# Optimization experiments

Hardware: AMD Instinct MI355X
Metric: run time of the kernel (lower is better)

The kernel has to match this reference:

```python
import jax, jax.numpy as jnp
import numpy as np

EMBED_DIM = 32  # module-level constant used for the 1/sqrt(d) scale in the source
DROP_P = 0.2


def setup_inputs() -> dict:
    key = jax.random.key(0)
    kx, kq, kk, kv = jax.random.split(key, 4)
    B, T, C = 8, 4096, EMBED_DIM
    x = jax.random.normal(kx, (B, T, C), dtype=jnp.float32)
    Wq = jax.random.normal(kq, (C, C), dtype=jnp.float32) * (1.0 / np.sqrt(C))
    Wk = jax.random.normal(kk, (C, C), dtype=jnp.float32) * (1.0 / np.sqrt(C))
    Wv = jax.random.normal(kv, (C, C), dtype=jnp.float32) * (1.0 / np.sqrt(C))
    return {"x": x, "Wq": Wq, "Wk": Wk, "Wv": Wv}


def reference(x, Wq, Wk, Wv):
    B, T, C = x.shape
    # bias-free linear projections: y = x @ W.T (torch nn.Linear convention)
    q = jnp.einsum('btc,dc->btd', x, Wq)
    k = jnp.einsum('btc,dc->btd', x, Wk)
    v = jnp.einsum('btc,dc->btd', x, Wv)
    # scaled scores [B, T, T]
    att = jnp.einsum('btd,bsd->bts', q, k) / jnp.sqrt(jnp.float32(EMBED_DIM))
    causal = jnp.tril(jnp.ones((T, T), dtype=bool))
    att = jnp.where(causal, att, -jnp.inf)
    wei = jax.nn.softmax(att, axis=-1)
    # dropout on attention weights (training mode, p=0.2), deterministic key
    keep = jax.random.bernoulli(jax.random.key(42), 1.0 - DROP_P, wei.shape)
    wei = jnp.where(keep, wei / (1.0 - DROP_P), 0.0)
    return jnp.einsum('bts,bsd->btd', wei, v)
```

## Files before the change

### kernel.cpp

```cpp
#include <hip/hip_runtime.h>
#include <stdint.h>

#define BB 8
#define TTN 4096
#define CCH 32
#define KEEP_LT9 3435974144u

typedef __attribute__((ext_vector_type(8))) short bf16x8;
typedef __attribute__((ext_vector_type(4))) float f32x4;

union B8 { uint32_t u[4]; uint4 q; bf16x8 v; };

__device__ __forceinline__ uint32_t cvt_pk_bf16(float lo, float hi) {
    uint32_t d;
    asm("v_cvt_pk_bf16_f32 %0, %1, %2" : "=v"(d) : "v"(lo), "v"(hi));
    return d;
}

__device__ __forceinline__ float exp2_fast(float x) {
    float d;
    asm("v_exp_f32 %0, %1" : "=v"(d) : "v"(x));
    return d;
}

__device__ __forceinline__ uint32_t rotl32(uint32_t x, int r) {
    return __builtin_amdgcn_alignbit(x, x, 32 - r);
}

__device__ __forceinline__ void threefry4(uint32_t i0, uint32_t i1, uint32_t i2, uint32_t i3,
                                          uint32_t& o0, uint32_t& o1, uint32_t& o2, uint32_t& o3) {
    const uint32_t K2 = 42u ^ 0x1BD11BDAu;
    uint32_t a0 = 0u, a1 = 0u, a2 = 0u, a3 = 0u;
    uint32_t b0 = i0 + 42u, b1 = i1 + 42u, b2 = i2 + 42u, b3 = i3 + 42u;
#define R4(r)                                                                  \
    { a0 += b0; a1 += b1; a2 += b2; a3 += b3;                                  \
      b0 = rotl32(b0, (r)); b1 = rotl32(b1, (r));                              \
      b2 = rotl32(b2, (r)); b3 = rotl32(b3, (r));                              \
      b0 ^= a0; b1 ^= a1; b2 ^= a2; b3 ^= a3; }
#define INJ(da, db)                                                            \
    { a0 += (da); a1 += (da); a2 += (da); a3 += (da);                          \
      b0 += (db); b1 += (db); b2 += (db); b3 += (db); }
    R4(13) R4(15) R4(26) R4(6)
    INJ(42u, K2 + 1u)
    R4(17) R4(29) R4(16) R4(24)
    INJ(K2, 2u)
    R4(13) R4(15) R4(26) R4(6)
    INJ(0u, 42u + 3u)
    R4(17) R4(29) R4(16) R4(24)
    INJ(42u, K2 + 4u)
    R4(13) R4(15) R4(26) R4(6)
    INJ(K2, 5u)
#undef R4
#undef INJ
    o0 = a0 ^ b0; o1 = a1 ^ b1; o2 = a2 ^ b2; o3 = a3 ^ b3;
}

__global__ __launch_bounds__(256) void proj_qkv(const float* __restrict__ x,
                                                const float* __restrict__ Wq,
                                                const float* __restrict__ Wk,
                                                const float* __restrict__ Wv,
                                                float* __restrict__ Qf,
                                                uint16_t* __restrict__ Kb,
                                                uint16_t* __restrict__ Vt) {
    __shared__ float sW[3][CCH * CCH];
    __shared__ uint16_t vs[256][34];
    const int tid = threadIdx.x;
    for (int i = tid; i < CCH * CCH; i += 256) {
        sW[0][i] = Wq[i]; sW[1][i] = Wk[i]; sW[2][i] = Wv[i];
    }
    __syncthreads();
    const int row = blockIdx.x * 256 + tid;
    const float4* xp = reinterpret_cast<const float4*>(x + (size_t)row * CCH);
    float xr[CCH];
    #pragma unroll
    for (int i = 0; i < 8; ++i) {
        float4 t4 = xp[i];
        xr[4*i] = t4.x; xr[4*i+1] = t4.y; xr[4*i+2] = t4.z; xr[4*i+3] = t4.w;
    }
    const float scale = 0.2550348616f;
    #pragma unroll
    for (int mtx = 0; mtx < 3; ++mtx) {
        float o[CCH];
        #pragma unroll
        for (int d = 0; d < CCH; ++d) {
            float s0 = 0.f, s1 = 0.f, s2 = 0.f, s3 = 0.f;
            #pragma unroll
            for (int c = 0; c < CCH; c += 4) {
                s0 += xr[c]   * sW[mtx][d*CCH + c];
                s1 += xr[c+1] * sW[mtx][d*CCH + c+1];
                s2 += xr[c+2] * sW[mtx][d*CCH + c+2];
                s3 += xr[c+3] * sW[mtx][d*CCH + c+3];
            }
            o[d] = (s0 + s1) + (s2 + s3);
            if (mtx == 0) o[d] *= scale;
        }
        if (mtx == 0) {
            float4* op = reinterpret_cast<float4*>(Qf + (size_t)row * CCH);
            #pragma unroll
            for (int i = 0; i < 8; ++i)
                op[i] = make_float4(o[4*i], o[4*i+1], o[4*i+2], o[4*i+3]);
        } else if (mtx == 1) {
            uint32_t dw[16];
            #pragma unroll
            for (int k = 0; k < 16; ++k) dw[k] = cvt_pk_bf16(o[2*k], o[2*k+1]);
            uint4* kp = reinterpret_cast<uint4*>((char*)Kb + (size_t)row * 64);
            #pragma unroll
            for (int q = 0; q < 4; ++q)
                kp[q] = make_uint4(dw[4*q], dw[4*q+1], dw[4*q+2], dw[4*q+3]);
        } else {
            #pragma unroll
            for (int k = 0; k < 16; ++k)
                *reinterpret_cast<uint32_t*>(&vs[tid][2*k]) = cvt_pk_bf16(o[2*k], o[2*k+1]);
        }
    }
    __syncthreads();
    const int b = blockIdx.x >> 4, seg = blockIdx.x & 15;
    const int d = tid >> 3, part = tid & 7;
    uint32_t dw[16];
    #pragma unroll
    for (int k = 0; k < 16; ++k) {
        const uint32_t lo = vs[part*32 + 2*k][d];
        const uint32_t hi = vs[part*32 + 2*k + 1][d];
        dw[k] = lo | (hi << 16);
    }
    uint16_t* dst = Vt + (size_t)b * (CCH * TTN) + (size_t)d * TTN + seg * 256 + part * 32;
    uint4* dp = reinterpret_cast<uint4*>(dst);
    #pragma unroll
    for (int q = 0; q < 4; ++q)
        dp[q] = make_uint4(dw[4*q], dw[4*q+1], dw[4*q+2], dw[4*q+3]);
}

__global__ __launch_bounds__(256, 6) void attn_mfma(const float* __restrict__ Qf,
                                                    const uint16_t* __restrict__ Kb,
                                                    const uint16_t* __restrict__ Vt,
                                                    float* __restrict__ out) {
    __shared__ __align__(16) char smem[9984];

    const int j = blockIdx.x;
    const int b = j & 7;
    const int thalf = (j >> 3) & 1;
    const int tile = 127 - (j >> 4);

    const int w = threadIdx.x >> 6;
    const int lane = threadIdx.x & 63;
    const int tl = lane & 15;
    const int g = lane >> 4;
    const int slb = w * 32;
    const int tbase = tile * 32 + thalf * 16;
    const int t_g = tbase + tl;

    const float* qrow = Qf + ((size_t)b * TTN + t_g) * CCH + g * 8;
    const float4 qa = *reinterpret_cast<const float4*>(qrow);
    const float4 qb = *reinterpret_cast<const float4*>(qrow + 4);
    B8 qf;
    qf.u[0] = cvt_pk_bf16(qa.x, qa.y); qf.u[1] = cvt_pk_bf16(qa.z, qa.w);
    qf.u[2] = cvt_pk_bf16(qb.x, qb.y); qf.u[3] = cvt_pk_bf16(qb.z, qb.w);

    f32x4 acc0 = {0.f,0.f,0.f,0.f}, acc1 = {0.f,0.f,0.f,0.f};
    float m = -1e30f, l = 0.f;

    const char* Kbb = (const char*)Kb + (size_t)b * TTN * 64;
    const char* Vbb = (const char*)Vt + (size_t)b * CCH * TTN * 2;
    const uint32_t idxb = ((uint32_t)b << 24) | ((uint32_t)t_g << 12);

    const int nwin = ((tbase + 15) >> 7) + 1;

    float* mxex = reinterpret_cast<float*>(smem) + (w << 6);
    uint32_t* pex = reinterpret_cast<uint32_t*>(smem + 1024) + (w << 8);

    B8 kaA, kcA, vaA, vcA, kaB, kcB, vaB, vcB;
    uint32_t rA[8], rB[8];

#define LOADF(KA, KC, VA, VC, S0)                                              \
    {                                                                          \
        const int srow = (S0) + slb;                                           \
        KA.q = *reinterpret_cast<const uint4*>(Kbb + (size_t)(srow + tl) * 64 + g * 16); \
        KC.q = *reinterpret_cast<const uint4*>(Kbb + (size_t)(srow + 16 + tl) * 64 + g * 16); \
        VA.q = *reinterpret_cast<const uint4*>(Vbb + (size_t)tl * 8192 + (size_t)(srow + g * 8) * 2); \
        VC.q = *reinterpret_cast<const uint4*>(Vbb + (size_t)(16 + tl) * 8192 + (size_t)(srow + g * 8) * 2); \
    }
#define TF8(R, S0)                                                             \
    {                                                                          \
        const uint32_t ib = idxb | (uint32_t)((S0) + slb + 4 * g);             \
        threefry4(ib,       ib + 1u,  ib + 2u,  ib + 3u,  R[0], R[1], R[2], R[3]); \
        threefry4(ib + 16u, ib + 17u, ib + 18u, ib + 19u, R[4], R[5], R[6], R[7]); \
    }
#define SMAXPV(S0, TAIL)                                                       \
    {                                                                          \
        const f32x4 zz = {0.f,0.f,0.f,0.f};                                    \
        f32x4 d0 = __builtin_amdgcn_mfma_f32_16x16x32_bf16(kaA.v, qf.v, zz, 0, 0, 0); \
        f32x4 d1 = __builtin_amdgcn_mfma_f32_16x16x32_bf16(kcA.v, qf.v, zz, 0, 0, 0); \
        if (TAIL) {                                                            \
            const int sv = (S0) + slb + 4 * g;                                 \
            d0.x = (sv + 0  <= t_g) ? d0.x : -1e30f;                           \
            d0.y = (sv + 1  <= t_g) ? d0.y : -1e30f;                           \
            d0.z = (sv + 2  <= t_g) ? d0.z : -1e30f;                           \
            d0.w = (sv + 3  <= t_g) ? d0.w : -1e30f;                           \
            d1.x = (sv + 16 <= t_g) ? d1.x : -1e30f;                           \
            d1.y = (sv + 17 <= t_g) ? d1.y : -1e30f;                           \
            d1.z = (sv + 18 <= t_g) ? d1.z : -1e30f;                           \
            d1.w = (sv + 19 <= t_g) ? d1.w : -1e30f;                           \
        }                                                                      \
        float mx = fmaxf(fmaxf(fmaxf(d0.x, d0.y), fmaxf(d0.z, d0.w)),          \
                         fmaxf(fmaxf(d1.x, d1.y), fmaxf(d1.z, d1.w)));         \
        mxex[(tl << 2) + g] = mx;                           \
        const float4 m4 = *reinterpret_cast<const float4*>(mxex + (tl << 2));  \
        mx = fmaxf(fmaxf(m4.x, m4.y), fmaxf(m4.z, m4.w));                      \
        const bool up = mx > m + 11.5f;          \
        const float corr = up ? exp2_fast(m - mx) : 1.0f;                      \
        m = up ? mx : m;                                                       \
        l *= corr; acc0 *= corr; acc1 *= corr;                                 \
        float p0 = exp2_fast(d0.x - m), p1 = exp2_fast(d0.y - m);              \
        float p2 = exp2_fast(d0.z - m), p3 = exp2_fast(d0.w - m);              \
        float p4 = exp2_fast(d1.x - m), p5 = exp2_fast(d1.y - m);              \
        float p6 = exp2_fast(d1.z - m), p7 = exp2_fast(d1.w - m);              \
        if (TAIL) {                                                            \
            const float alive = ((S0) + slb <= t_g) ? 1.0f : 0.0f;             \
            p0 *= alive; p1 *= alive; p2 *= alive; p3 *= alive;                \
            p4 *= alive; p5 *= alive; p6 *= alive; p7 *= alive;                \
        }                                                                      \
        l += ((p0 + p1) + (p2 + p3)) + ((p4 + p5) + (p6 + p7));                \
        const float q0 = (rA[0] < KEEP_LT9) ? p0 : 0.f;                        \
        const float q1 = (rA[1] < KEEP_LT9) ? p1 : 0.f;                        \
        const float q2 = (rA[2] < KEEP_LT9) ? p2 : 0.f;                        \
        const float q3 = (rA[3] < KEEP_LT9) ? p3 : 0.f;                        \
        const float q4 = (rA[4] < KEEP_LT9) ? p4 : 0.f;                        \
        const float q5 = (rA[5] < KEEP_LT9) ? p5 : 0.f;                        \
        const float q6 = (rA[6] < KEEP_LT9) ? p6 : 0.f;                        \
        const float q7 = (rA[7] < KEEP_LT9) ? p7 : 0.f;                        \
        const uint32_t k00 = cvt_pk_bf16(q0, q1), k01 = cvt_pk_bf16(q2, q3);   \
        const uint32_t k10 = cvt_pk_bf16(q4, q5), k11 = cvt_pk_bf16(q6, q7);   \
        *reinterpret_cast<uint4*>(pex + (lane << 2)) = make_uint4(k00, k01, k10, k11); \
        const int srcA4 = (((g & 1) ? 32 : 0) + tl) << 2;                      \
        const int sel = (g >= 2) ? 2 : 0;                                      \
        const uint2 lo2 = *reinterpret_cast<const uint2*>(pex + srcA4 + sel);  \
        const uint2 hi2 = *reinterpret_cast<const uint2*>(pex + srcA4 + 64 + sel); \
        B8 pf;                                                                 \
        pf.u[0] = lo2.x; pf.u[1] = lo2.y; pf.u[2] = hi2.x; pf.u[3] = hi2.y;    \
        acc0 = __builtin_amdgcn_mfma_f32_16x16x32_bf16(vaA.v, pf.v, acc0, 0, 0, 0); \
        acc1 = __builtin_amdgcn_mfma_f32_16x16x32_bf16(vcA.v, pf.v, acc1, 0, 0, 0); \
    }

    LOADF(kaA, kcA, vaA, vcA, 0)
    TF8(rA, 0)
    #pragma unroll 1
    for (int win = 0; win < nwin - 1; ++win) {
        LOADF(kaB, kcB, vaB, vcB, (win + 1) << 7)
        TF8(rB, (win + 1) << 7)
        SMAXPV(win << 7, 0)
        kaA = kaB; kcA = kcB; vaA = vaB; vcA = vcB;
        #pragma unroll
        for (int i = 0; i < 8; ++i) rA[i] = rB[i];
    }
    {
        const int s0 = (nwin - 1) << 7;
        if (s0 + slb <= tbase + 15) SMAXPV(s0, 1)
    }
#undef SMAXPV
#undef TF8
#undef LOADF

    l += __shfl_xor(l, 16);
    l += __shfl_xor(l, 32);

#define SLOT(S) reinterpret_cast<float*>(smem + 5120 + (S) * 2432)
#define PUBLISH(SB)                                                            \
    {                                                                          \
        float* sb = (SB);                                                      \
        *reinterpret_cast<float4*>(sb + tl * 36 + 4 * g)      = make_float4(acc0.x, acc0.y, acc0.z, acc0.w); \
        *reinterpret_cast<float4*>(sb + tl * 36 + 16 + 4 * g) = make_float4(acc1.x, acc1.y, acc1.z, acc1.w); \
        if (g == 0) { sb[576 + 2 * tl] = m; sb[577 + 2 * tl] = l; }            \
    }
#define CONSUME(SB)                                                            \
    {                                                                          \
        const float* sb = (SB);                                                \
        const float m2 = sb[576 + 2 * tl], l2 = sb[577 + 2 * tl];              \
        const float4 x0 = *reinterpret_cast<const float4*>(sb + tl * 36 + 4 * g); \
        const float4 x1 = *reinterpret_cast<const float4*>(sb + tl * 36 + 16 + 4 * g); \
        const float mn = fmaxf(m, m2);                                         \
        const float ca = exp2_fast(m - mn), cb = exp2_fast(m2 - mn);           \
        l = l * ca + l2 * cb;                                                  \
        acc0.x = acc0.x * ca + x0.x * cb; acc0.y = acc0.y * ca + x0.y * cb;    \
        acc0.z = acc0.z * ca + x0.z * cb; acc0.w = acc0.w * ca + x0.w * cb;    \
        acc1.x = acc1.x * ca + x1.x * cb; acc1.y = acc1.y * ca + x1.y * cb;    \
        acc1.z = acc1.z * ca + x1.z * cb; acc1.w = acc1.w * ca + x1.w * cb;    \
        m = mn;                                                                \
    }
    if (w >= 2) PUBLISH(SLOT(w - 2))
    __syncthreads();
    if (w < 2) CONSUME(SLOT(w))
    __syncthreads();
    if (w == 1) PUBLISH(SLOT(0))
    __syncthreads();
    if (w == 0) {
        CONSUME(SLOT(0))
        const float inv = 1.0f / (0.8f * l);
        float* orow = out + ((size_t)b * TTN + t_g) * CCH;
        *reinterpret_cast<float4*>(orow + 4 * g) =
            make_float4(acc0.x * inv, acc0.y * inv, acc0.z * inv, acc0.w * inv);
        *reinterpret_cast<float4*>(orow + 16 + 4 * g) =
            make_float4(acc1.x * inv, acc1.y * inv, acc1.z * inv, acc1.w * inv);
    }
#undef SLOT
#undef PUBLISH
#undef CONSUME
}

extern "C" void kernel_launch(void* const* d_in, const int* in_sizes, int n_in,
                              void* d_out, int out_size, void* d_ws, size_t ws_size,
                              hipStream_t stream) {
    const float* x  = (const float*)d_in[0];
    const float* Wq = (const float*)d_in[1];
    const float* Wk = (const float*)d_in[2];
    const float* Wv = (const float*)d_in[3];
    float* outp = (float*)d_out;

    float*    Qf = (float*)d_ws;
    uint16_t* Kb = (uint16_t*)((char*)d_ws + 4194304);
    uint16_t* Vt = (uint16_t*)((char*)d_ws + 6291456);

    proj_qkv<<<(BB * TTN) / 256, 256, 0, stream>>>(x, Wq, Wk, Wv, Qf, Kb, Vt);
    attn_mfma<<<2048, 256, 0, stream>>>(Qf, Kb, Vt, outp);
}
```

Measured before the change: 164.7 us.

## Split KV windows across two segments, pair causal tiles per block, add merge kernel

```diff
diff --git a/kernel.cpp b/kernel.cpp
--- a/kernel.cpp
+++ b/kernel.cpp
@@ -130,46 +130,51 @@
         dp[q] = make_uint4(dw[4*q], dw[4*q+1], dw[4*q+2], dw[4*q+3]);
 }
 
-__global__ __launch_bounds__(256, 6) void attn_mfma(const float* __restrict__ Qf,
+__global__ __launch_bounds__(256, 8) void attn_mfma(const float* __restrict__ Qf,
                                                     const uint16_t* __restrict__ Kb,
                                                     const uint16_t* __restrict__ Vt,
-                                                    float* __restrict__ out) {
+                                                    float* __restrict__ pws) {
     __shared__ __align__(16) char smem[9984];
 
     const int j = blockIdx.x;
     const int b = j & 7;
-    const int thalf = (j >> 3) & 1;
-    const int tile = 127 - (j >> 4);
+    const int p = (j >> 3) & 63;
+    const int h = (j >> 9) & 1;
+    const int seg = (j >> 10) & 1;
 
     const int w = threadIdx.x >> 6;
     const int lane = threadIdx.x & 63;
     const int tl = lane & 15;
     const int g = lane >> 4;
     const int slb = w * 32;
-    const int tbase = tile * 32 + thalf * 16;
-    const int t_g = tbase + tl;
-
-    const float* qrow = Qf + ((size_t)b * TTN + t_g) * CCH + g * 8;
-    const float4 qa = *reinterpret_cast<const float4*>(qrow);
-    const float4 qb = *reinterpret_cast<const float4*>(qrow + 4);
-    B8 qf;
-    qf.u[0] = cvt_pk_bf16(qa.x, qa.y); qf.u[1] = cvt_pk_bf16(qa.z, qa.w);
-    qf.u[2] = cvt_pk_bf16(qb.x, qb.y); qf.u[3] = cvt_pk_bf16(qb.z, qb.w);
-
-    f32x4 acc0 = {0.f,0.f,0.f,0.f}, acc1 = {0.f,0.f,0.f,0.f};
-    float m = -1e30f, l = 0.f;
 
     const char* Kbb = (const char*)Kb + (size_t)b * TTN * 64;
     const char* Vbb = (const char*)Vt + (size_t)b * CCH * TTN * 2;
-    const uint32_t idxb = ((uint32_t)b << 24) | ((uint32_t)t_g << 12);
-
-    const int nwin = ((tbase + 15) >> 7) + 1;
 
     float* mxex = reinterpret_cast<float*>(smem) + (w << 6);
     uint32_t* pex = reinterpret_cast<uint32_t*>(smem + 1024) + (w << 8);
 
-    B8 kaA, kcA, vaA, vcA, kaB, kcB, vaB, vcB;
-    uint32_t rA[8], rB[8];
+    #pragma unroll 1
+    for (int leg = 0; leg < 2; ++leg) {
+        const int tile = leg ? (127 - p) : p;
+        const int th = leg ? (1 - h) : h;
+        const int tbase = tile * 32 + th * 16;
+        const int t_g = tbase + tl;
+        const int nwin = ((tbase + 15) >> 7) + 1;
+        const uint32_t idxb = ((uint32_t)b << 24) | ((uint32_t)t_g << 12);
+
+        const float* qrow = Qf + ((size_t)b * TTN + t_g) * CCH + g * 8;
+        const float4 qa = *reinterpret_cast<const float4*>(qrow);
+        const float4 qb = *reinterpret_cast<const float4*>(qrow + 4);
+        B8 qf;
+        qf.u[0] = cvt_pk_bf16(qa.x, qa.y); qf.u[1] = cvt_pk_bf16(qa.z, qa.w);
+        qf.u[2] = cvt_pk_bf16(qb.x, qb.y); qf.u[3] = cvt_pk_bf16(qb.z, qb.w);
+
+        f32x4 acc0 = {0.f,0.f,0.f,0.f}, acc1 = {0.f,0.f,0.f,0.f};
+        float m = -1e30f, l = 0.f;
+
+        B8 kaA, kcA, vaA, vcA, kaB, kcB, vaB, vcB;
+        uint32_t rA[8], rB[8];
 
 #define LOADF(KA, KC, VA, VC, S0)                                              \
     {                                                                          \
@@ -185,12 +190,13 @@
         threefry4(ib,       ib + 1u,  ib + 2u,  ib + 3u,  R[0], R[1], R[2], R[3]); \
         threefry4(ib + 16u, ib + 17u, ib + 18u, ib + 19u, R[4], R[5], R[6], R[7]); \
     }
-#define SMAXPV(S0, TAIL)                                                       \
+#define SMAXPV(KA, KC, VA, VC, R, S0, ISTAIL)                                  \
     {                                                                          \
         const f32x4 zz = {0.f,0.f,0.f,0.f};                                    \
-        f32x4 d0 = __builtin_amdgcn_mfma_f32_16x16x32_bf16(kaA.v, qf.v, zz, 0, 0, 0); \
-        f32x4 d1 = __builtin_amdgcn_mfma_f32_16x16x32_bf16(kcA.v, qf.v, zz, 0, 0, 0); \
-        if (TAIL) {                                                            \
+        f32x4 d0 = __builtin_amdgcn_mfma_f32_16x16x32_bf16(KA.v, qf.v, zz, 0, 0, 0); \
+        f32x4 d1 = __builtin_amdgcn_mfma_f32_16x16x32_bf16(KC.v, qf.v, zz, 0, 0, 0); \
+        const bool istail_ = (ISTAIL);                                         \
+        if (istail_) {                                                         \
             const int sv = (S0) + slb + 4 * g;                                 \
             d0.x = (sv + 0  <= t_g) ? d0.x : -1e30f;                           \
             d0.y = (sv + 1  <= t_g) ? d0.y : -1e30f;                           \
@@ -203,10 +209,10 @@
         }                                                                      \
         float mx = fmaxf(fmaxf(fmaxf(d0.x, d0.y), fmaxf(d0.z, d0.w)),          \
                          fmaxf(fmaxf(d1.x, d1.y), fmaxf(d1.z, d1.w)));         \
-        mxex[(tl << 2) + g] = mx;                           \
+        mxex[(tl << 2) + g] = mx;                                              \
         const float4 m4 = *reinterpret_cast<const float4*>(mxex + (tl << 2));  \
         mx = fmaxf(fmaxf(m4.x, m4.y), fmaxf(m4.z, m4.w));                      \
-        const bool up = mx > m + 11.5f;          \
+        const bool up = mx > m + 11.5f;                                        \
         const float corr = up ? exp2_fast(m - mx) : 1.0f;                      \
         m = up ? mx : m;                                                       \
         l *= corr; acc0 *= corr; acc1 *= corr;                                 \
@@ -214,20 +220,20 @@
         float p2 = exp2_fast(d0.z - m), p3 = exp2_fast(d0.w - m);              \
         float p4 = exp2_fast(d1.x - m), p5 = exp2_fast(d1.y - m);              \
         float p6 = exp2_fast(d1.z - m), p7 = exp2_fast(d1.w - m);              \
-        if (TAIL) {                                                            \
+        if (istail_) {                                                         \
             const float alive = ((S0) + slb <= t_g) ? 1.0f : 0.0f;             \
             p0 *= alive; p1 *= alive; p2 *= alive; p3 *= alive;                \
             p4 *= alive; p5 *= alive; p6 *= alive; p7 *= alive;                \
         }                                                                      \
         l += ((p0 + p1) + (p2 + p3)) + ((p4 + p5) + (p6 + p7));                \
-        const float q0 = (rA[0] < KEEP_LT9) ? p0 : 0.f;                        \
-        const float q1 = (rA[1] < KEEP_LT9) ? p1 : 0.f;                        \
-        const float q2 = (rA[2] < KEEP_LT9) ? p2 : 0.f;                        \
-        const float q3 = (rA[3] < KEEP_LT9) ? p3 : 0.f;                        \
-        const float q4 = (rA[4] < KEEP_LT9) ? p4 : 0.f;                        \
-        const float q5 = (rA[5] < KEEP_LT9) ? p5 : 0.f;                        \
-        const float q6 = (rA[6] < KEEP_LT9) ? p6 : 0.f;                        \
-        const float q7 = (rA[7] < KEEP_LT9) ? p7 : 0.f;                        \
+        const float q0 = (R[0] < KEEP_LT9) ? p0 : 0.f;                         \
+        const float q1 = (R[1] < KEEP_LT9) ? p1 : 0.f;                         \
+        const float q2 = (R[2] < KEEP_LT9) ? p2 : 0.f;                         \
+        const float q3 = (R[3] < KEEP_LT9) ? p3 : 0.f;                         \
+        const float q4 = (R[4] < KEEP_LT9) ? p4 : 0.f;                         \
+        const float q5 = (R[5] < KEEP_LT9) ? p5 : 0.f;                         \
+        const float q6 = (R[6] < KEEP_LT9) ? p6 : 0.f;                         \
+        const float q7 = (R[7] < KEEP_LT9) ? p7 : 0.f;                         \
         const uint32_t k00 = cvt_pk_bf16(q0, q1), k01 = cvt_pk_bf16(q2, q3);   \
         const uint32_t k10 = cvt_pk_bf16(q4, q5), k11 = cvt_pk_bf16(q6, q7);   \
         *reinterpret_cast<uint4*>(pex + (lane << 2)) = make_uint4(k00, k01, k10, k11); \
@@ -237,31 +243,42 @@
         const uint2 hi2 = *reinterpret_cast<const uint2*>(pex + srcA4 + 64 + sel); \
         B8 pf;                                                                 \
         pf.u[0] = lo2.x; pf.u[1] = lo2.y; pf.u[2] = hi2.x; pf.u[3] = hi2.y;    \
-        acc0 = __builtin_amdgcn_mfma_f32_16x16x32_bf16(vaA.v, pf.v, acc0, 0, 0, 0); \
-        acc1 = __builtin_amdgcn_mfma_f32_16x16x32_bf16(vcA.v, pf.v, acc1, 0, 0, 0); \
-    }
-
-    LOADF(kaA, kcA, vaA, vcA, 0)
-    TF8(rA, 0)
-    #pragma unroll 1
-    for (int win = 0; win < nwin - 1; ++win) {
-        LOADF(kaB, kcB, vaB, vcB, (win + 1) << 7)
-        TF8(rB, (win + 1) << 7)
-        SMAXPV(win << 7, 0)
-        kaA = kaB; kcA = kcB; vaA = vaB; vcA = vcB;
-        #pragma unroll
-        for (int i = 0; i < 8; ++i) rA[i] = rB[i];
-    }
-    {
-        const int s0 = (nwin - 1) << 7;
-        if (s0 + slb <= tbase + 15) SMAXPV(s0, 1)
-    }
+        acc0 = __builtin_amdgcn_mfma_f32_16x16x32_bf16(VA.v, pf.v, acc0, 0, 0, 0); \
+        acc1 = __builtin_amdgcn_mfma_f32_16x16x32_bf16(VC.v, pf.v, acc1, 0, 0, 0); \
+    }
+
+        int win = seg;
+        if (win < nwin) {
+            LOADF(kaA, kcA, vaA, vcA, win << 7)
+            TF8(rA, win << 7)
+            while (true) {
+                int nxt = win + 2;
+                if (nxt < nwin) {
+                    LOADF(kaB, kcB, vaB, vcB, nxt << 7)
+                    TF8(rB, nxt << 7)
+                    SMAXPV(kaA, kcA, vaA, vcA, rA, win << 7, win == nwin - 1)
+                } else {
+                    SMAXPV(kaA, kcA, vaA, vcA, rA, win << 7, win == nwin - 1)
+                    break;
+                }
+                win = nxt; nxt = win + 2;
+                if (nxt < nwin) {
+                    LOADF(kaA, kcA, vaA, vcA, nxt << 7)
+                    TF8(rA, nxt << 7)
+                    SMAXPV(kaB, kcB, vaB, vcB, rB, win << 7, win == nwin - 1)
+                } else {
+                    SMAXPV(kaB, kcB, vaB, vcB, rB, win << 7, win == nwin - 1)
+                    break;
+                }
+                win = nxt;
+            }
+        }
 #undef SMAXPV
 #undef TF8
 #undef LOADF
 
-    l += __shfl_xor(l, 16);
-    l += __shfl_xor(l, 32);
+        l += __shfl_xor(l, 16);
+        l += __shfl_xor(l, 32);
 
 #define SLOT(S) reinterpret_cast<float*>(smem + 5120 + (S) * 2432)
 #define PUBLISH(SB)                                                            \
@@ -286,24 +303,57 @@
         acc1.z = acc1.z * ca + x1.z * cb; acc1.w = acc1.w * ca + x1.w * cb;    \
         m = mn;                                                                \
     }
-    if (w >= 2) PUBLISH(SLOT(w - 2))
-    __syncthreads();
-    if (w < 2) CONSUME(SLOT(w))
-    __syncthreads();
-    if (w == 1) PUBLISH(SLOT(0))
-    __syncthreads();
-    if (w == 0) {
-        CONSUME(SLOT(0))
-        const float inv = 1.0f / (0.8f * l);
-        float* orow = out + ((size_t)b * TTN + t_g) * CCH;
-        *reinterpret_cast<float4*>(orow + 4 * g) =
-            make_float4(acc0.x * inv, acc0.y * inv, acc0.z * inv, acc0.w * inv);
-        *reinterpret_cast<float4*>(orow + 16 + 4 * g) =
-            make_float4(acc1.x * inv, acc1.y * inv, acc1.z * inv, acc1.w * inv);
-    }
+        __syncthreads();
+        if (w >= 2) PUBLISH(SLOT(w - 2))
+        __syncthreads();
+        if (w < 2) CONSUME(SLOT(w))
+        __syncthreads();
+        if (w == 1) PUBLISH(SLOT(0))
+        __syncthreads();
+        if (w == 0) {
+            CONSUME(SLOT(0))
+            const int gi = (b << 8) + (tile << 1) + th;
+            float* dst = pws + (((size_t)gi * 2 + seg) * 16 + tl) * 34;
+            if (g == 0) { dst[0] = m; dst[1] = l; }
+            *reinterpret_cast<float4*>(dst + 2 + 4 * g) =
+                make_float4(acc0.x, acc0.y, acc0.z, acc0.w);
+            *reinterpret_cast<float4*>(dst + 18 + 4 * g) =
+                make_float4(acc1.x, acc1.y, acc1.z, acc1.w);
+        }
+        __syncthreads();
 #undef SLOT
 #undef PUBLISH
 #undef CONSUME
+    }
+}
+
+__global__ __launch_bounds__(256) void merge_out(const float* __restrict__ pws,
+                                                 float* __restrict__ out) {
+    const int gw = (blockIdx.x << 2) + (threadIdx.x >> 6);
+    const int lane = threadIdx.x & 63;
+    const int tl = lane & 15, g = lane >> 4;
+    const int b = gw >> 8, tile = (gw & 255) >> 1, th = gw & 1;
+
+    const float* s0 = pws + (((size_t)gw * 2 + 0) * 16 + tl) * 34;
+    const float* s1 = pws + (((size_t)gw * 2 + 1) * 16 + tl) * 34;
+    const float m0 = s0[0], l0 = s0[1], m1 = s1[0], l1 = s1[1];
+    const float mn = fmaxf(m0, m1);
+    const float c0 = exp2_fast(m0 - mn);
+    const float c1 = exp2_fast(m1 - mn);
+    const float inv = 1.0f / (0.8f * (l0 * c0 + l1 * c1));
+
+    const float4 a0 = *reinterpret_cast<const float4*>(s0 + 2 + 4 * g);
+    const float4 b0 = *reinterpret_cast<const float4*>(s1 + 2 + 4 * g);
+    const float4 a1 = *reinterpret_cast<const float4*>(s0 + 18 + 4 * g);
+    const float4 b1 = *reinterpret_cast<const float4*>(s1 + 18 + 4 * g);
+
+    float* orow = out + (((size_t)b * TTN) + tile * 32 + th * 16 + tl) * CCH;
+    *reinterpret_cast<float4*>(orow + 4 * g) = make_float4(
+        (a0.x * c0 + b0.x * c1) * inv, (a0.y * c0 + b0.y * c1) * inv,
+        (a0.z * c0 + b0.z * c1) * inv, (a0.w * c0 + b0.w * c1) * inv);
+    *reinterpret_cast<float4*>(orow + 16 + 4 * g) = make_float4(
+        (a1.x * c0 + b1.x * c1) * inv, (a1.y * c0 + b1.y * c1) * inv,
+        (a1.z * c0 + b1.z * c1) * inv, (a1.w * c0 + b1.w * c1) * inv);
 }
 
 extern "C" void kernel_launch(void* const* d_in, const int* in_sizes, int n_in,
@@ -315,10 +365,12 @@
     const float* Wv = (const float*)d_in[3];
     float* outp = (float*)d_out;
 
-    float*    Qf = (float*)d_ws;
-    uint16_t* Kb = (uint16_t*)((char*)d_ws + 4194304);
-    uint16_t* Vt = (uint16_t*)((char*)d_ws + 6291456);
+    float*    Qf  = (float*)d_ws;
+    uint16_t* Kb  = (uint16_t*)((char*)d_ws + 4194304);
+    uint16_t* Vt  = (uint16_t*)((char*)d_ws + 6291456);
+    float*    pws = (float*)((char*)d_ws + 8388608);
 
     proj_qkv<<<(BB * TTN) / 256, 256, 0, stream>>>(x, Wq, Wk, Wv, Qf, Kb, Vt);
-    attn_mfma<<<2048, 256, 0, stream>>>(Qf, Kb, Vt, outp);
-}
+    attn_mfma<<<2048, 256, 0, stream>>>(Qf, Kb, Vt, pws);
+    merge_out<<<512, 256, 0, stream>>>(pws, outp);
+}
```

Result: slower. 428.0 us (+160.0%).
